# Kernel optimization log

Hardware: AMD Instinct MI355X
Metric: run time of the kernel (lower is better)

## Reference

```python
import jax, jax.numpy as jnp
import numpy as np

N = 100_000   # nodes
E = 3_200_000 # edges
B = 64        # graphs in batch
OUT = 64      # config


def setup_inputs() -> dict:
    key = jax.random.key(0)
    ks = jax.random.split(key, 12)
    x = jax.random.normal(ks[0], (N, 3), dtype=jnp.float32)
    edge_index = jax.random.randint(ks[1], (2, E), 0, N, dtype=jnp.int32)
    batch = jnp.sort(jax.random.randint(ks[2], (N,), 0, B, dtype=jnp.int32))
    # GCNConv weights (PyG: out = norm_adj @ (x @ W) + b)
    W1 = jax.random.normal(ks[3], (3, 32), dtype=jnp.float32) * 0.5
    b1 = jnp.zeros((32,), dtype=jnp.float32)
    W2 = jax.random.normal(ks[4], (32, 32), dtype=jnp.float32) * 0.18
    b2 = jnp.zeros((32,), dtype=jnp.float32)
    LW1 = jax.random.normal(ks[5], (64, 64), dtype=jnp.float32) * 0.125
    Lb1 = jnp.zeros((64,), dtype=jnp.float32)
    LW2 = jax.random.normal(ks[6], (64, OUT), dtype=jnp.float32) * 0.125
    Lb2 = jnp.zeros((OUT,), dtype=jnp.float32)
    return {"x": x, "edge_index": edge_index, "batch": batch,
            "W1": W1, "b1": b1, "W2": W2, "b2": b2,
            "LW1": LW1, "Lb1": Lb1, "LW2": LW2, "Lb2": Lb2}


def _gcn_norm(edge_index, n):
    # add self-loops, compute symmetric normalization D^-1/2 (A+I) D^-1/2
    loops = jnp.arange(n, dtype=edge_index.dtype)
    src = jnp.concatenate([edge_index[0], loops])
    dst = jnp.concatenate([edge_index[1], loops])
    deg = jax.ops.segment_sum(jnp.ones_like(dst, dtype=jnp.float32), dst,
                              num_segments=n)
    dinv = jnp.where(deg > 0, 1.0 / jnp.sqrt(deg), 0.0)
    norm = dinv[src] * dinv[dst]  # [E+N]
    return src, dst, norm


def _gcn_conv(x, W, b, src, dst, norm, n):
    h = x @ W                         # [N, F_out] tiny GEMM
    m = h[src] * norm[:, None]        # edge gather  [E+N, F_out]
    out = jax.ops.segment_sum(m, dst, num_segments=n)  # scatter-add
    return out + b


def _pool(x, batch, nb):
    # cat(global_max_pool, global_mean_pool)
    mx = jax.ops.segment_max(x, batch, num_segments=nb)
    sm = jax.ops.segment_sum(x, batch, num_segments=nb)
    cnt = jax.ops.segment_sum(jnp.ones((x.shape[0],), x.dtype), batch,
                              num_segments=nb)
    mean = sm / jnp.maximum(cnt, 1.0)[:, None]
    return jnp.concatenate([mx, mean], axis=1)


def reference(x, edge_index, batch, W1, b1, W2, b2, LW1, Lb1, LW2, Lb2):
    n = x.shape[0]
    src, dst, norm = _gcn_norm(edge_index, n)
    h = jax.nn.relu(_gcn_conv(x, W1, b1, src, dst, norm, n))
    x1 = _pool(h, batch, B)           # [B, 64]
    h2 = jax.nn.relu(_gcn_conv(h, W2, b2, src, dst, norm, n))
    x2 = _pool(h2, batch, B)          # [B, 64]
    z = jax.nn.relu((x1 + x2) @ LW1 + Lb1)
    # dropout p=0.5 skipped (eval mode / training=False)
    out = z @ LW2 + Lb2               # [B, OUT]; .squeeze(1) is a no-op for OUT>1
    return out
```

## Files before the change

kernel.cpp:

```cpp
#include <hip/hip_runtime.h>
#include <hip/hip_fp16.h>


#define F 32
#define POOLD 64
#define BKT 512
#define BKTL2 9
#define EPB 8192
#define MAXBUCK 256

typedef __attribute__((ext_vector_type(8))) _Float16 half8;

__global__ void k_histB(const int* __restrict__ ei, int* __restrict__ bcnt,
                        int e, int nbuck, int nblk) {
    __shared__ int h[MAXBUCK];
    for (int b = threadIdx.x; b < nbuck; b += 256) h[b] = 0;
    __syncthreads();
    int base = blockIdx.x * EPB;
#pragma unroll
    for (int k = 0; k < EPB / 1024; ++k) {
        int i = base + (k * 256 + threadIdx.x) * 4;
        if (i + 4 <= e) {
            int4 d4 = *reinterpret_cast<const int4*>(ei + e + i);
            atomicAdd(&h[d4.x >> BKTL2], 1);
            atomicAdd(&h[d4.y >> BKTL2], 1);
            atomicAdd(&h[d4.z >> BKTL2], 1);
            atomicAdd(&h[d4.w >> BKTL2], 1);
        } else {
            for (int j = i; j < e && j < i + 4; ++j)
                atomicAdd(&h[ei[e + j] >> BKTL2], 1);
        }
    }
    __syncthreads();
    for (int b = threadIdx.x; b < nbuck; b += 256)
        bcnt[b * nblk + blockIdx.x] = h[b];
}

__global__ void k_rowscan(int* __restrict__ bcnt, int* __restrict__ tot, int nblk) {
    __shared__ int lds[256];
    int* row = bcnt + (size_t)blockIdx.x * nblk;
    int t = threadIdx.x;
    int running = 0;
    for (int chunk = 0; chunk < nblk; chunk += 256) {
        int idx = chunk + t;
        int v = (idx < nblk) ? row[idx] : 0;
        lds[t] = v;
        __syncthreads();
        int val = v;
        for (int off = 1; off < 256; off <<= 1) {
            int other = (t >= off) ? lds[t - off] : 0;
            __syncthreads();
            val += other;
            lds[t] = val;
            __syncthreads();
        }
        if (idx < nblk) row[idx] = running + val - v;
        running += lds[255];
        __syncthreads();
    }
    if (t == 0) tot[blockIdx.x] = running;
}

__global__ void k_bscan(const int* __restrict__ tot, int* __restrict__ bstart,
                        int nbuck, int e) {
    __shared__ int lds[256];
    int t = threadIdx.x;
    int v = (t < nbuck) ? tot[t] : 0;
    lds[t] = v;
    __syncthreads();
    int val = v;
    for (int off = 1; off < 256; off <<= 1) {
        int other = (t >= off) ? lds[t - off] : 0;
        __syncthreads();
        val += other;
        lds[t] = val;
        __syncthreads();
    }
    if (t < nbuck) bstart[t] = val - v;
    if (t == 0) bstart[nbuck] = e;
}

__global__ void k_bin(const int* __restrict__ ei, const int* __restrict__ bstart,
                      const int* __restrict__ bcnt, int* __restrict__ packed,
                      int e, int nbuck, int nblk) {
    __shared__ int cur[MAXBUCK];
    for (int b = threadIdx.x; b < nbuck; b += 256)
        cur[b] = bstart[b] + bcnt[b * nblk + blockIdx.x];
    __syncthreads();
    int base = blockIdx.x * EPB;
#pragma unroll
    for (int k = 0; k < EPB / 1024; ++k) {
        int i = base + (k * 256 + threadIdx.x) * 4;
        if (i + 4 <= e) {
            int4 s4 = *reinterpret_cast<const int4*>(ei + i);
            int4 d4 = *reinterpret_cast<const int4*>(ei + e + i);
            int p0 = atomicAdd(&cur[d4.x >> BKTL2], 1);
            int p1 = atomicAdd(&cur[d4.y >> BKTL2], 1);
            int p2 = atomicAdd(&cur[d4.z >> BKTL2], 1);
            int p3 = atomicAdd(&cur[d4.w >> BKTL2], 1);
            packed[p0] = (s4.x << BKTL2) | (d4.x & (BKT - 1));
            packed[p1] = (s4.y << BKTL2) | (d4.y & (BKT - 1));
            packed[p2] = (s4.z << BKTL2) | (d4.z & (BKT - 1));
            packed[p3] = (s4.w << BKTL2) | (d4.w & (BKT - 1));
        } else {
            for (int j = i; j < e && j < i + 4; ++j) {
                int s = ei[j], d = ei[e + j];
                int p = atomicAdd(&cur[d >> BKTL2], 1);
                packed[p] = (s << BKTL2) | (d & (BKT - 1));
            }
        }
    }
}

__global__ void k_place2(const int* __restrict__ packed, const int* __restrict__ bstart,
                         int* __restrict__ col, int* __restrict__ rp,
                         float* __restrict__ dinv, int n) {
    __shared__ int deg[BKT];
    __shared__ int sc[BKT];
    __shared__ int cur[BKT];
    int t = threadIdx.x;
    deg[t] = 0;
    __syncthreads();
    int start = bstart[blockIdx.x];
    int end = bstart[blockIdx.x + 1];
    for (int i = start + t; i < end; i += BKT)
        atomicAdd(&deg[packed[i] & (BKT - 1)], 1);
    __syncthreads();
    int d0 = deg[t];
    sc[t] = d0;
    __syncthreads();
    int val = d0;
    for (int off = 1; off < BKT; off <<= 1) {
        int other = (t >= off) ? sc[t - off] : 0;
        __syncthreads();
        val += other;
        sc[t] = val;
        __syncthreads();
    }
    int node = blockIdx.x * BKT + t;
    int ex = start + val - d0;
    if (node < n) {
        rp[node] = ex;
        dinv[node] = rsqrtf((float)d0 + 1.0f);
    }
    cur[t] = ex;
    __syncthreads();
    for (int i = start + t; i < end; i += BKT) {
        int u = packed[i];
        int p = atomicAdd(&cur[u & (BKT - 1)], 1);
        col[p] = u >> BKTL2;
    }
}

__global__ void k_xw1(const float* __restrict__ x, const float* __restrict__ W1,
                      _Float16* __restrict__ p0, _Float16* __restrict__ p1, int n) {
    int i = blockIdx.x * blockDim.x + threadIdx.x;
    if (i >= n * F) return;
    int node = i >> 5, f = i & (F - 1);
    float x0 = x[node * 3 + 0], x1 = x[node * 3 + 1], x2 = x[node * 3 + 2];
    float v = x0 * W1[f] + x1 * W1[F + f] + x2 * W1[2 * F + f];
    _Float16* plane = (f < 16) ? p0 : p1;
    plane[node * 16 + (f & 15)] = (_Float16)v;
}

__global__ void k_gemm2(const _Float16* __restrict__ h0, const _Float16* __restrict__ h1,
                        const float* __restrict__ W2,
                        _Float16* __restrict__ g0, _Float16* __restrict__ g1, int n) {
    int i = blockIdx.x * blockDim.x + threadIdx.x;
    if (i >= n * F) return;
    int node = i >> 5, f = i & (F - 1);
    const _Float16* r0 = h0 + (size_t)node * 16;
    const _Float16* r1 = h1 + (size_t)node * 16;
    float acc = 0.0f;
#pragma unroll
    for (int k = 0; k < 16; ++k) acc += (float)r0[k] * W2[k * F + f];
#pragma unroll
    for (int k = 0; k < 16; ++k) acc += (float)r1[k] * W2[(k + 16) * F + f];
    _Float16* plane = (f < 16) ? g0 : g1;
    plane[node * 16 + (f & 15)] = (_Float16)acc;
}

__global__ void k_gather2(const _Float16* __restrict__ pl0, const _Float16* __restrict__ pl1,
                          const int* __restrict__ rp, const int* __restrict__ col,
                          const float* __restrict__ dinv, const float* __restrict__ bias,
                          const int* __restrict__ batch,
                          _Float16* __restrict__ out0, _Float16* __restrict__ out1,
                          float* __restrict__ psum, float* __restrict__ pmax,
                          float* __restrict__ cnt, int n, int ne, int nPB,
                          int store, int do_cnt) {
    int grp = blockIdx.x >> 3, sub = blockIdx.x & 7;
    int plane = sub >> 2;
    int lb = grp * 4 + (sub & 3);
    if (lb >= nPB) return;
    int t = threadIdx.x;
    int node = (lb << 6) + (t >> 2);
    int q = (t >> 1) & 1, r = t & 1;
    if (node >= n) return;

    const _Float16* hin = plane ? pl1 : pl0;
    int start = rp[node];
    int end = (node + 1 < n) ? rp[node + 1] : ne;
    float dv = dinv[node];

    float acc[8];
    {
        half8 hv = *reinterpret_cast<const half8*>(hin + (size_t)node * 16 + q * 8);
        float dvv = (r == 0) ? dv * dv : 0.0f;
#pragma unroll
        for (int j = 0; j < 8; ++j) acc[j] = (float)hv[j] * dvv;
    }

    int e = start + r;
    for (; e + 6 < end; e += 8) {
        int s0 = col[e], s1 = col[e + 2], s2 = col[e + 4], s3 = col[e + 6];
        half8 v0 = *reinterpret_cast<const half8*>(hin + (size_t)s0 * 16 + q * 8);
        half8 v1 = *reinterpret_cast<const half8*>(hin + (size_t)s1 * 16 + q * 8);
        half8 v2 = *reinterpret_cast<const half8*>(hin + (size_t)s2 * 16 + q * 8);
        half8 v3 = *reinterpret_cast<const half8*>(hin + (size_t)s3 * 16 + q * 8);
        float w0 = dinv[s0] * dv, w1 = dinv[s1] * dv,
              w2 = dinv[s2] * dv, w3 = dinv[s3] * dv;
#pragma unroll
        for (int j = 0; j < 8; ++j)
            acc[j] += (float)v0[j] * w0 + (float)v1[j] * w1 +
                      (float)v2[j] * w2 + (float)v3[j] * w3;
    }
    for (; e < end; e += 2) {
        int s = col[e];
        float wv = dinv[s] * dv;
        half8 v = *reinterpret_cast<const half8*>(hin + (size_t)s * 16 + q * 8);
#pragma unroll
        for (int j = 0; j < 8; ++j) acc[j] += (float)v[j] * wv;
    }

#pragma unroll
    for (int j = 0; j < 8; ++j) acc[j] += __shfl_xor(acc[j], 1);

    float vv[8];
#pragma unroll
    for (int j = 0; j < 8; ++j)
        vv[j] = fmaxf(acc[j] + bias[plane * 16 + q * 8 + j], 0.0f);

    if (store && r == 0) {
        _Float16* hout = plane ? out1 : out0;
        half8 o;
#pragma unroll
        for (int j = 0; j < 8; ++j) o[j] = (_Float16)vv[j];
        *reinterpret_cast<half8*>(hout + (size_t)node * 16 + q * 8) = o;
    }

    int b = batch[node];
    int lane = t & 63;
    int bFirst = __shfl(b, 0);
    int bLast  = __shfl(b, 63);
    if (bFirst == bLast) {
        float sv[8], mv[8];
#pragma unroll
        for (int j = 0; j < 8; ++j) { sv[j] = vv[j]; mv[j] = vv[j]; }
        for (int off = 4; off < 64; off <<= 1) {
#pragma unroll
            for (int j = 0; j < 8; ++j) {
                sv[j] += __shfl_down(sv[j], off);
                mv[j] = fmaxf(mv[j], __shfl_down(mv[j], off));
            }
        }
        if (lane < 4 && r == 0) {
            float* ps = psum + b * F + plane * 16 + q * 8;
            int* pm = reinterpret_cast<int*>(pmax + b * F + plane * 16 + q * 8);
#pragma unroll
            for (int j = 0; j < 8; ++j) {
                atomicAdd(ps + j, sv[j]);
                atomicMax(pm + j, __float_as_int(mv[j]));
            }
            if (do_cnt && plane == 0 && lane == 0) atomicAdd(&cnt[b], 16.0f);
        }
    } else if (r == 0) {
        float* ps = psum + b * F + plane * 16 + q * 8;
        int* pm = reinterpret_cast<int*>(pmax + b * F + plane * 16 + q * 8);
#pragma unroll
        for (int j = 0; j < 8; ++j) {
            atomicAdd(ps + j, vv[j]);
            atomicMax(pm + j, __float_as_int(vv[j]));
        }
        if (do_cnt && plane == 0 && q == 0) atomicAdd(&cnt[b], 1.0f);
    }
}

__global__ void k_mlp(const float* __restrict__ sum1, const float* __restrict__ max1,
                      const float* __restrict__ sum2, const float* __restrict__ max2,
                      const float* __restrict__ cnt,
                      const float* __restrict__ LW1, const float* __restrict__ Lb1,
                      const float* __restrict__ LW2, const float* __restrict__ Lb2,
                      float* __restrict__ out, int outd) {
    __shared__ float zs[POOLD];
    int b = blockIdx.x, j = threadIdx.x;
    float invc = 1.0f / fmaxf(cnt[b], 1.0f);
    float acc = Lb1[j];
#pragma unroll
    for (int i = 0; i < POOLD; ++i) {
        float s;
        if (i < F) s = max1[b * F + i] + max2[b * F + i];
        else       s = (sum1[b * F + i - F] + sum2[b * F + i - F]) * invc;
        acc += s * LW1[i * POOLD + j];
    }
    zs[j] = fmaxf(acc, 0.0f);
    __syncthreads();
    if (j < outd) {
        float a2 = Lb2[j];
#pragma unroll
        for (int jj = 0; jj < POOLD; ++jj) a2 += zs[jj] * LW2[jj * outd + j];
        out[b * outd + j] = a2;
    }
}

extern "C" void kernel_launch(void* const* d_in, const int* in_sizes, int n_in,
                              void* d_out, int out_size, void* d_ws, size_t ws_size,
                              hipStream_t stream) {
    const float* x    = (const float*)d_in[0];
    const int*   ei   = (const int*)d_in[1];
    const int*   batch= (const int*)d_in[2];
    const float* W1   = (const float*)d_in[3];
    const float* b1   = (const float*)d_in[4];
    const float* W2   = (const float*)d_in[5];
    const float* b2   = (const float*)d_in[6];
    const float* LW1  = (const float*)d_in[7];
    const float* Lb1  = (const float*)d_in[8];
    const float* LW2  = (const float*)d_in[9];
    const float* Lb2  = (const float*)d_in[10];
    float* out = (float*)d_out;

    const int N = in_sizes[0] / 3;
    const int E = in_sizes[1] / 2;
    const int OUTD = in_sizes[10];
    const int B = out_size / OUTD;
    const int poolsz = 4 * B * F + B;
    const int NBUCK = (N + BKT - 1) / BKT;
    const int NBLK = (E + EPB - 1) / EPB;
    const int NPB = (N + 63) / 64;

    char* p = (char*)d_ws;
    float* pools= (float*)p;          p += (size_t)poolsz * 4;
    int* bcnt   = (int*)p;            p += (size_t)NBUCK * NBLK * 4;
    int* tot    = (int*)p;            p += (size_t)MAXBUCK * 4;
    int* bstart = (int*)p;            p += (size_t)(NBUCK + 1) * 4;
    int* rowptr = (int*)p;            p += (size_t)N * 4;
    int* col    = (int*)p;            p += (size_t)E * 4;
    float* dinv = (float*)p;          p += (size_t)N * 4;
    _Float16* b0p0 = (_Float16*)p;    p += (size_t)N * 16 * 2;
    _Float16* b0p1 = (_Float16*)p;    p += (size_t)N * 16 * 2;
    _Float16* b1p0 = (_Float16*)p;    p += (size_t)N * 16 * 2;
    _Float16* b1p1 = (_Float16*)p;    p += (size_t)N * 16 * 2;
    int* packed = (int*)b0p0;
    float* sum1 = pools;
    float* max1 = sum1 + B * F;
    float* sum2 = max1 + B * F;
    float* max2 = sum2 + B * F;
    float* cnt  = max2 + B * F;

    const int BS = 256;
    auto g1 = [&](long long n) { return (int)((n + BS - 1) / BS); };
    const int gatherBlocks = ((NPB + 3) / 4) * 8;

    hipMemsetAsync(pools, 0, (size_t)poolsz * 4, stream);
    k_histB<<<NBLK, BS, 0, stream>>>(ei, bcnt, E, NBUCK, NBLK);
    k_rowscan<<<NBUCK, 256, 0, stream>>>(bcnt, tot, NBLK);
    k_bscan<<<1, 256, 0, stream>>>(tot, bstart, NBUCK, E);
    k_bin<<<NBLK, BS, 0, stream>>>(ei, bstart, bcnt, packed, E, NBUCK, NBLK);
    k_place2<<<NBUCK, BKT, 0, stream>>>(packed, bstart, col, rowptr, dinv, N);

    k_xw1<<<g1((long long)N * F), BS, 0, stream>>>(x, W1, b0p0, b0p1, N);
    k_gather2<<<gatherBlocks, BS, 0, stream>>>(b0p0, b0p1, rowptr, col, dinv, b1,
                                               batch, b1p0, b1p1, sum1, max1, cnt,
                                               N, E, NPB, 1, 1);
    k_gemm2<<<g1((long long)N * F), BS, 0, stream>>>(b1p0, b1p1, W2, b0p0, b0p1, N);
    k_gather2<<<gatherBlocks, BS, 0, stream>>>(b0p0, b0p1, rowptr, col, dinv, b2,
                                               batch, b1p0, b1p1, sum2, max2, cnt,
                                               N, E, NPB, 0, 0);

    k_mlp<<<B, 64, 0, stream>>>(sum1, max1, sum2, max2, cnt,
                                LW1, Lb1, LW2, Lb2, out, OUTD);
}
```

Baseline: 369.1 us.

## Pre-scale features by dinv and split each node's edges across 8 lanes

Folds the source-side D^-1/2 factor into the feature transforms (xW1 and hW2 now multiply by dinv[node]), so the gather no longer loads dinv[src] per edge and applies only the destination scale once at the end. The gather kernel is restructured so each node gets 8 lanes. Each lane handles a contiguous slice of the edge list, reads both 16-wide half8 halves per neighbour, and the lanes are combined with an xor-shuffle reduction. This removes the per-edge random dinv load and changes memory access granularity, at the cost of more registers (16 accumulators) and an extra fp16 rounding of the pre-scaled features.

```diff
diff --git a/kernel.cpp b/kernel.cpp
--- a/kernel.cpp
+++ b/kernel.cpp
@@ -153,18 +153,19 @@
 }
 
 __global__ void k_xw1(const float* __restrict__ x, const float* __restrict__ W1,
+                      const float* __restrict__ dinv,
                       _Float16* __restrict__ p0, _Float16* __restrict__ p1, int n) {
     int i = blockIdx.x * blockDim.x + threadIdx.x;
     if (i >= n * F) return;
     int node = i >> 5, f = i & (F - 1);
     float x0 = x[node * 3 + 0], x1 = x[node * 3 + 1], x2 = x[node * 3 + 2];
-    float v = x0 * W1[f] + x1 * W1[F + f] + x2 * W1[2 * F + f];
+    float v = (x0 * W1[f] + x1 * W1[F + f] + x2 * W1[2 * F + f]) * dinv[node];
     _Float16* plane = (f < 16) ? p0 : p1;
     plane[node * 16 + (f & 15)] = (_Float16)v;
 }
 
 __global__ void k_gemm2(const _Float16* __restrict__ h0, const _Float16* __restrict__ h1,
-                        const float* __restrict__ W2,
+                        const float* __restrict__ W2, const float* __restrict__ dinv,
                         _Float16* __restrict__ g0, _Float16* __restrict__ g1, int n) {
     int i = blockIdx.x * blockDim.x + threadIdx.x;
     if (i >= n * F) return;
@@ -177,10 +178,10 @@
 #pragma unroll
     for (int k = 0; k < 16; ++k) acc += (float)r1[k] * W2[(k + 16) * F + f];
     _Float16* plane = (f < 16) ? g0 : g1;
-    plane[node * 16 + (f & 15)] = (_Float16)acc;
-}
-
-__global__ void k_gather2(const _Float16* __restrict__ pl0, const _Float16* __restrict__ pl1,
+    plane[node * 16 + (f & 15)] = (_Float16)(acc * dinv[node]);
+}
+
+__global__ void k_gather3(const _Float16* __restrict__ pl0, const _Float16* __restrict__ pl1,
                           const int* __restrict__ rp, const int* __restrict__ col,
                           const float* __restrict__ dinv, const float* __restrict__ bias,
                           const int* __restrict__ batch,
@@ -193,59 +194,71 @@
     int lb = grp * 4 + (sub & 3);
     if (lb >= nPB) return;
     int t = threadIdx.x;
-    int node = (lb << 6) + (t >> 2);
-    int q = (t >> 1) & 1, r = t & 1;
+    int node = (lb << 5) + (t >> 3);
+    int rr = t & 7;
     if (node >= n) return;
 
     const _Float16* hin = plane ? pl1 : pl0;
     int start = rp[node];
     int end = (node + 1 < n) ? rp[node + 1] : ne;
+    int len = end - start;
+    int m0 = start + ((len * rr) >> 3);
+    int m1 = start + ((len * (rr + 1)) >> 3);
     float dv = dinv[node];
 
-    float acc[8];
-    {
-        half8 hv = *reinterpret_cast<const half8*>(hin + (size_t)node * 16 + q * 8);
-        float dvv = (r == 0) ? dv * dv : 0.0f;
-#pragma unroll
-        for (int j = 0; j < 8; ++j) acc[j] = (float)hv[j] * dvv;
-    }
-
-    int e = start + r;
-    for (; e + 6 < end; e += 8) {
-        int s0 = col[e], s1 = col[e + 2], s2 = col[e + 4], s3 = col[e + 6];
-        half8 v0 = *reinterpret_cast<const half8*>(hin + (size_t)s0 * 16 + q * 8);
-        half8 v1 = *reinterpret_cast<const half8*>(hin + (size_t)s1 * 16 + q * 8);
-        half8 v2 = *reinterpret_cast<const half8*>(hin + (size_t)s2 * 16 + q * 8);
-        half8 v3 = *reinterpret_cast<const half8*>(hin + (size_t)s3 * 16 + q * 8);
-        float w0 = dinv[s0] * dv, w1 = dinv[s1] * dv,
-              w2 = dinv[s2] * dv, w3 = dinv[s3] * dv;
-#pragma unroll
-        for (int j = 0; j < 8; ++j)
-            acc[j] += (float)v0[j] * w0 + (float)v1[j] * w1 +
-                      (float)v2[j] * w2 + (float)v3[j] * w3;
-    }
-    for (; e < end; e += 2) {
+    float acc[16];
+    if (rr == 0) {
+        half8 a = *reinterpret_cast<const half8*>(hin + (size_t)node * 16);
+        half8 b = *reinterpret_cast<const half8*>(hin + (size_t)node * 16 + 8);
+#pragma unroll
+        for (int j = 0; j < 8; ++j) { acc[j] = (float)a[j]; acc[8 + j] = (float)b[j]; }
+    } else {
+#pragma unroll
+        for (int j = 0; j < 16; ++j) acc[j] = 0.0f;
+    }
+
+    int e = m0;
+    for (; e + 4 <= m1; e += 4) {
+        int s0 = col[e], s1 = col[e + 1], s2 = col[e + 2], s3 = col[e + 3];
+        half8 a0 = *reinterpret_cast<const half8*>(hin + (size_t)s0 * 16);
+        half8 b0 = *reinterpret_cast<const half8*>(hin + (size_t)s0 * 16 + 8);
+        half8 a1 = *reinterpret_cast<const half8*>(hin + (size_t)s1 * 16);
+        half8 b1 = *reinterpret_cast<const half8*>(hin + (size_t)s1 * 16 + 8);
+        half8 a2 = *reinterpret_cast<const half8*>(hin + (size_t)s2 * 16);
+        half8 b2 = *reinterpret_cast<const half8*>(hin + (size_t)s2 * 16 + 8);
+        half8 a3 = *reinterpret_cast<const half8*>(hin + (size_t)s3 * 16);
+        half8 b3 = *reinterpret_cast<const half8*>(hin + (size_t)s3 * 16 + 8);
+#pragma unroll
+        for (int j = 0; j < 8; ++j) {
+            acc[j]     += (float)a0[j] + (float)a1[j] + (float)a2[j] + (float)a3[j];
+            acc[8 + j] += (float)b0[j] + (float)b1[j] + (float)b2[j] + (float)b3[j];
+        }
+    }
+    for (; e < m1; ++e) {
         int s = col[e];
-        float wv = dinv[s] * dv;
-        half8 v = *reinterpret_cast<const half8*>(hin + (size_t)s * 16 + q * 8);
-#pragma unroll
-        for (int j = 0; j < 8; ++j) acc[j] += (float)v[j] * wv;
-    }
-
-#pragma unroll
-    for (int j = 0; j < 8; ++j) acc[j] += __shfl_xor(acc[j], 1);
-
-    float vv[8];
-#pragma unroll
-    for (int j = 0; j < 8; ++j)
-        vv[j] = fmaxf(acc[j] + bias[plane * 16 + q * 8 + j], 0.0f);
-
-    if (store && r == 0) {
+        half8 a = *reinterpret_cast<const half8*>(hin + (size_t)s * 16);
+        half8 b = *reinterpret_cast<const half8*>(hin + (size_t)s * 16 + 8);
+#pragma unroll
+        for (int j = 0; j < 8; ++j) { acc[j] += (float)a[j]; acc[8 + j] += (float)b[j]; }
+    }
+
+#pragma unroll
+    for (int off = 1; off < 8; off <<= 1)
+#pragma unroll
+        for (int j = 0; j < 16; ++j) acc[j] += __shfl_xor(acc[j], off);
+
+    float vv[16];
+#pragma unroll
+    for (int j = 0; j < 16; ++j)
+        vv[j] = fmaxf(dv * acc[j] + bias[plane * 16 + j], 0.0f);
+
+    if (store && rr == 0) {
         _Float16* hout = plane ? out1 : out0;
-        half8 o;
-#pragma unroll
-        for (int j = 0; j < 8; ++j) o[j] = (_Float16)vv[j];
-        *reinterpret_cast<half8*>(hout + (size_t)node * 16 + q * 8) = o;
+        half8 oa, ob;
+#pragma unroll
+        for (int j = 0; j < 8; ++j) { oa[j] = (_Float16)vv[j]; ob[j] = (_Float16)vv[8 + j]; }
+        *reinterpret_cast<half8*>(hout + (size_t)node * 16) = oa;
+        *reinterpret_cast<half8*>(hout + (size_t)node * 16 + 8) = ob;
     }
 
     int b = batch[node];
@@ -253,35 +266,35 @@
     int bFirst = __shfl(b, 0);
     int bLast  = __shfl(b, 63);
     if (bFirst == bLast) {
-        float sv[8], mv[8];
-#pragma unroll
-        for (int j = 0; j < 8; ++j) { sv[j] = vv[j]; mv[j] = vv[j]; }
-        for (int off = 4; off < 64; off <<= 1) {
-#pragma unroll
-            for (int j = 0; j < 8; ++j) {
+        float sv[16], mv[16];
+#pragma unroll
+        for (int j = 0; j < 16; ++j) { sv[j] = vv[j]; mv[j] = vv[j]; }
+        for (int off = 8; off < 64; off <<= 1) {
+#pragma unroll
+            for (int j = 0; j < 16; ++j) {
                 sv[j] += __shfl_down(sv[j], off);
                 mv[j] = fmaxf(mv[j], __shfl_down(mv[j], off));
             }
         }
-        if (lane < 4 && r == 0) {
-            float* ps = psum + b * F + plane * 16 + q * 8;
-            int* pm = reinterpret_cast<int*>(pmax + b * F + plane * 16 + q * 8);
+        if (lane < 2) {
+            float* ps = psum + b * F + plane * 16 + lane * 8;
+            int* pm = reinterpret_cast<int*>(pmax + b * F + plane * 16 + lane * 8);
 #pragma unroll
             for (int j = 0; j < 8; ++j) {
-                atomicAdd(ps + j, sv[j]);
-                atomicMax(pm + j, __float_as_int(mv[j]));
+                atomicAdd(ps + j, sv[lane * 8 + j]);
+                atomicMax(pm + j, __float_as_int(mv[lane * 8 + j]));
             }
-            if (do_cnt && plane == 0 && lane == 0) atomicAdd(&cnt[b], 16.0f);
-        }
-    } else if (r == 0) {
-        float* ps = psum + b * F + plane * 16 + q * 8;
-        int* pm = reinterpret_cast<int*>(pmax + b * F + plane * 16 + q * 8);
-#pragma unroll
-        for (int j = 0; j < 8; ++j) {
+            if (do_cnt && plane == 0 && lane == 0) atomicAdd(&cnt[b], 8.0f);
+        }
+    } else if (rr == 0) {
+        float* ps = psum + b * F + plane * 16;
+        int* pm = reinterpret_cast<int*>(pmax + b * F + plane * 16);
+#pragma unroll
+        for (int j = 0; j < 16; ++j) {
             atomicAdd(ps + j, vv[j]);
             atomicMax(pm + j, __float_as_int(vv[j]));
         }
-        if (do_cnt && plane == 0 && q == 0) atomicAdd(&cnt[b], 1.0f);
+        if (do_cnt && plane == 0) atomicAdd(&cnt[b], 1.0f);
     }
 }
 
@@ -335,7 +348,7 @@
     const int poolsz = 4 * B * F + B;
     const int NBUCK = (N + BKT - 1) / BKT;
     const int NBLK = (E + EPB - 1) / EPB;
-    const int NPB = (N + 63) / 64;
+    const int NPB = (N + 31) / 32;
 
     char* p = (char*)d_ws;
     float* pools= (float*)p;          p += (size_t)poolsz * 4;
@@ -367,12 +380,13 @@
     k_bin<<<NBLK, BS, 0, stream>>>(ei, bstart, bcnt, packed, E, NBUCK, NBLK);
     k_place2<<<NBUCK, BKT, 0, stream>>>(packed, bstart, col, rowptr, dinv, N);
 
-    k_xw1<<<g1((long long)N * F), BS, 0, stream>>>(x, W1, b0p0, b0p1, N);
-    k_gather2<<<gatherBlocks, BS, 0, stream>>>(b0p0, b0p1, rowptr, col, dinv, b1,
+    k_xw1<<<g1((long long)N * F), BS, 0, stream>>>(x, W1, dinv, b0p0, b0p1, N);
+    k_gather3<<<gatherBlocks, BS, 0, stream>>>(b0p0, b0p1, rowptr, col, dinv, b1,
                                                batch, b1p0, b1p1, sum1, max1, cnt,
                                                N, E, NPB, 1, 1);
-    k_gemm2<<<g1((long long)N * F), BS, 0, stream>>>(b1p0, b1p1, W2, b0p0, b0p1, N);
-    k_gather2<<<gatherBlocks, BS, 0, stream>>>(b0p0, b0p1, rowptr, col, dinv, b2,
+    k_gemm2<<<g1((long long)N * F), BS, 0, stream>>>(b1p0, b1p1, W2, dinv,
+                                                     b0p0, b0p1, N);
+    k_gather3<<<gatherBlocks, BS, 0, stream>>>(b0p0, b0p1, rowptr, col, dinv, b2,
                                                batch, b1p0, b1p1, sum2, max2, cnt,
                                                N, E, NPB, 0, 0);
 
```

Result: slower. 455.4 us (+23.4%).
